# Kernel optimization log

Hardware: AMD Instinct MI355X
Metric: run time of the kernel (lower is better)

Reference implementation:

```python
import jax, jax.numpy as jnp
import numpy as np

TEMPERATURE = 0.7
BIG_NEG = -1e30  # safe stand-in for -inf (keeps grads finite)


def setup_inputs() -> dict:
    key = jax.random.key(0)
    k1, k2, k3 = jax.random.split(key, 3)
    B, D = 8192, 256
    embeddings = jax.random.normal(k1, (B, D), dtype=jnp.float32)
    categories = jax.random.randint(k2, (B,), 0, 16, dtype=jnp.int64)
    font_labels = jax.random.randint(k3, (B,), 0, 2000, dtype=jnp.int64)
    return {"embeddings": embeddings, "categories": categories, "font_labels": font_labels}


def reference(embeddings, categories, font_labels):
    # L2-normalize rows
    e = embeddings / jnp.linalg.norm(embeddings, axis=1, keepdims=True)
    sims = jnp.matmul(e, e.T) / TEMPERATURE  # [B, B]
    B = sims.shape[0]

    same = categories[:, None] == categories[None, :]
    diag = jnp.eye(B, dtype=bool)
    pos_mask = same & ~diag           # same category, excluding self
    neg_mask = ~same                  # different category (self excluded implicitly)

    valid = pos_mask.any(axis=1) & neg_mask.any(axis=1)

    pos_sim = jnp.max(jnp.where(pos_mask, sims, BIG_NEG), axis=1)  # hardest positive per anchor
    neg_max = jnp.max(jnp.where(neg_mask, sims, BIG_NEG), axis=1)

    # logsumexp over {pos_sim} U neg_sims, numerically stable
    m = jnp.where(valid, jnp.maximum(pos_sim, neg_max), 0.0)
    pos_safe = jnp.where(valid, pos_sim, 0.0)
    exp_neg_sum = jnp.sum(jnp.where(neg_mask, jnp.exp(sims - m[:, None]), 0.0), axis=1)
    lse = m + jnp.log(jnp.exp(pos_safe - m) + exp_neg_sum)

    loss_per_anchor = -pos_safe + lse
    n_valid = jnp.maximum(jnp.sum(valid), 1)
    return jnp.sum(jnp.where(valid, loss_per_anchor, 0.0)) / n_valid
```

## Files before the change

### kernel.cpp

```cpp
#include <hip/hip_runtime.h>
#include <stdint.h>

#define NROWS 8192
#define DDIM 256
#define NSTRIPS 32
#define STRIP_COLS 256
#define BN 32
#define NTILES 8
#define BM 128
#define NSLOT NSTRIPS

#define ESCALE 1.4356159f
#define LN2F   0.6931471806f
#define NEGBIG (-1e30f)

typedef __attribute__((ext_vector_type(8))) short short8;
typedef __attribute__((ext_vector_type(4))) float f32x4;

__device__ __forceinline__ unsigned short f2bf(float x) {
  unsigned int u = __float_as_uint(x);
  u += 0x7fffu + ((u >> 16) & 1u);
  return (unsigned short)(u >> 16);
}

__global__ __launch_bounds__(256) void knorm(const float* __restrict__ emb,
                                             unsigned short* __restrict__ ebf,
                                             unsigned short* __restrict__ ebfB,
                                             uint4* __restrict__ accv) {
  if (blockIdx.x == 0 && threadIdx.x == 0) *accv = (uint4){0u, 0u, 0u, 0u};
  const int wave = threadIdx.x >> 6, lane = threadIdx.x & 63;
  const int row = blockIdx.x * 4 + wave;
  const float4 v = *(const float4*)(emb + row * DDIM + lane * 4);
  float ss = v.x * v.x + v.y * v.y + v.z * v.z + v.w * v.w;
#pragma unroll
  for (int off = 1; off < 64; off <<= 1) ss += __shfl_xor(ss, off, 64);
  const float sc = rsqrtf(ss) * ESCALE;
  ushort4 o;
  o.x = f2bf(v.x * sc); o.y = f2bf(v.y * sc);
  o.z = f2bf(v.z * sc); o.w = f2bf(v.w * sc);
  *(ushort4*)(ebf + row * DDIM + lane * 4) = o;
  *(ushort4*)(ebfB + ((lane >> 1) * NROWS + row) * 8 + (lane & 1) * 4) = o;
}

__global__ __launch_bounds__(256) void kmain(const unsigned short* __restrict__ ebf,
                                             const unsigned short* __restrict__ ebfB,
                                             const int* __restrict__ cats,
                                             float* __restrict__ posP,
                                             float* __restrict__ sumP) {
  const int tid = threadIdx.x;
  const int lane = tid & 63, wave = tid >> 6;
  const int lane15 = lane & 15, quad = lane >> 4;
  const int strip = blockIdx.x, rowTile = blockIdx.y;
  const int rowG = rowTile * BM + wave * 32;
  const int col0 = strip * STRIP_COLS;

  short8 a[2][8];
#pragma unroll
  for (int m = 0; m < 2; ++m)
#pragma unroll
    for (int kk = 0; kk < 8; ++kk)
      a[m][kk] = *(const short8*)(ebf + (rowG + m * 16 + lane15) * DDIM + kk * 32 + quad * 8);

  int cati[2][4];
#pragma unroll
  for (int m = 0; m < 2; ++m)
#pragma unroll
    for (int r = 0; r < 4; ++r)
      cati[m][r] = cats[rowG + m * 16 + quad * 4 + r];

  bool dlr[4];
#pragma unroll
  for (int r = 0; r < 4; ++r) dlr[r] = (lane15 == quad * 4 + r);

  float pm[2][4], ns[2][4];
#pragma unroll
  for (int m = 0; m < 2; ++m)
#pragma unroll
    for (int r = 0; r < 4; ++r) { pm[m][r] = NEGBIG; ns[m][r] = 0.f; }

  const unsigned short* bbase = ebfB + ((size_t)quad * NROWS + col0 + lane15) * 8;

  for (int t = 0; t < NTILES; ++t) {
#pragma unroll
    for (int nt = 0; nt < 2; ++nt) {
      const int colBase = col0 + t * BN + nt * 16;
      short8 b[8];
#pragma unroll
      for (int kk = 0; kk < 8; ++kk)
        b[kk] = *(const short8*)(bbase + ((size_t)kk * 4 * NROWS + t * BN + nt * 16) * 8);
      f32x4 acc0 = {0.f, 0.f, 0.f, 0.f}, acc1 = {0.f, 0.f, 0.f, 0.f};
      __builtin_amdgcn_s_setprio(1);
#pragma unroll
      for (int kk = 0; kk < 8; ++kk) {
        acc0 = __builtin_amdgcn_mfma_f32_16x16x32_bf16(a[0][kk], b[kk], acc0, 0, 0, 0);
        acc1 = __builtin_amdgcn_mfma_f32_16x16x32_bf16(a[1][kk], b[kk], acc1, 0, 0, 0);
      }
      __builtin_amdgcn_s_setprio(0);
      const int cj = cats[colBase + lane15];
      const bool dg0 = (rowG == colBase);
      const bool dg1 = (rowG + 16 == colBase);
#pragma unroll
      for (int m = 0; m < 2; ++m) {
        const bool dg = m ? dg1 : dg0;
#pragma unroll
        for (int r = 0; r < 4; ++r) {
          const float s = m ? acc1[r] : acc0[r];
          const float e = __builtin_amdgcn_exp2f(s);
          const bool same = (cj == cati[m][r]);
          float psv = same ? s : NEGBIG;
          if (dg) psv = dlr[r] ? NEGBIG : psv;
          pm[m][r] = fmaxf(pm[m][r], psv);
          ns[m][r] += same ? 0.f : e;
        }
      }
    }
  }

#pragma unroll
  for (int off = 1; off < 16; off <<= 1) {
#pragma unroll
    for (int m = 0; m < 2; ++m)
#pragma unroll
      for (int r = 0; r < 4; ++r) {
        pm[m][r] = fmaxf(pm[m][r], __shfl_xor(pm[m][r], off, 64));
        ns[m][r] += __shfl_xor(ns[m][r], off, 64);
      }
  }
  if (lane15 == 0) {
#pragma unroll
    for (int m = 0; m < 2; ++m)
#pragma unroll
      for (int r = 0; r < 4; ++r) {
        const int row = rowG + m * 16 + quad * 4 + r;
        posP[strip * NROWS + row] = pm[m][r];
        sumP[strip * NROWS + row] = ns[m][r];
      }
  }
}

__global__ __launch_bounds__(256) void kmerge(const float* __restrict__ posP,
                                              const float* __restrict__ sumP,
                                              float* __restrict__ acc,
                                              float* __restrict__ out) {
  const int row = blockIdx.x * 256 + threadIdx.x;
  float pm = NEGBIG, ns = 0.f;
#pragma unroll 8
  for (int s = 0; s < NSLOT; ++s) {
    pm = fmaxf(pm, posP[s * NROWS + row]);
    ns += sumP[s * NROWS + row];
  }
  const bool valid = (pm > -1e29f) && (ns > 0.f);
  float loss = valid ? (logf(__builtin_amdgcn_exp2f(pm) + ns) - pm * LN2F) : 0.f;
  float cnt = valid ? 1.f : 0.f;
#pragma unroll
  for (int off = 1; off < 64; off <<= 1) {
    loss += __shfl_xor(loss, off, 64);
    cnt += __shfl_xor(cnt, off, 64);
  }
  if ((threadIdx.x & 63) == 0) {
    atomicAdd(&acc[0], loss);
    atomicAdd(&acc[1], cnt);
    __threadfence();
  }
  __syncthreads();
  if (threadIdx.x == 0) {
    const int prev = atomicAdd((int*)(acc + 2), 1);
    if (prev == (int)gridDim.x - 1) {
      const float L = atomicAdd(&acc[0], 0.f);
      const float C = atomicAdd(&acc[1], 0.f);
      out[0] = L / fmaxf(C, 1.f);
    }
  }
}

extern "C" void kernel_launch(void* const* d_in, const int* in_sizes, int n_in,
                              void* d_out, int out_size, void* d_ws, size_t ws_size,
                              hipStream_t stream) {
  const float* emb = (const float*)d_in[0];
  const int* cats = (const int*)d_in[1];
  float* out = (float*)d_out;

  char* ws = (char*)d_ws;
  float* accv = (float*)ws;
  unsigned short* ebf = (unsigned short*)(ws + 256);
  unsigned short* ebfB = ebf + (size_t)NROWS * DDIM;
  float* posP = (float*)(ws + 256 + 2 * (size_t)NROWS * DDIM * 2);
  float* sumP = posP + NSLOT * NROWS;

  knorm<<<NROWS / 4, 256, 0, stream>>>(emb, ebf, ebfB, (uint4*)ws);
  kmain<<<dim3(NSTRIPS, NROWS / BM), 256, 0, stream>>>(ebf, ebfB, cats, posP, sumP);
  kmerge<<<NROWS / 256, 256, 0, stream>>>(posP, sumP, accv, out);
}
```

Baseline: 121.1 us.

## Double-buffer B fragment loads and drop row-major bf16 copy

```diff
diff --git a/kernel.cpp b/kernel.cpp
--- a/kernel.cpp
+++ b/kernel.cpp
@@ -24,7 +24,6 @@
 }
 
 __global__ __launch_bounds__(256) void knorm(const float* __restrict__ emb,
-                                             unsigned short* __restrict__ ebf,
                                              unsigned short* __restrict__ ebfB,
                                              uint4* __restrict__ accv) {
   if (blockIdx.x == 0 && threadIdx.x == 0) *accv = (uint4){0u, 0u, 0u, 0u};
@@ -38,18 +37,17 @@
   ushort4 o;
   o.x = f2bf(v.x * sc); o.y = f2bf(v.y * sc);
   o.z = f2bf(v.z * sc); o.w = f2bf(v.w * sc);
-  *(ushort4*)(ebf + row * DDIM + lane * 4) = o;
   *(ushort4*)(ebfB + ((lane >> 1) * NROWS + row) * 8 + (lane & 1) * 4) = o;
 }
 
-__global__ __launch_bounds__(256) void kmain(const unsigned short* __restrict__ ebf,
-                                             const unsigned short* __restrict__ ebfB,
+__global__ __launch_bounds__(256) void kmain(const unsigned short* __restrict__ ebfB,
                                              const int* __restrict__ cats,
                                              float* __restrict__ posP,
                                              float* __restrict__ sumP) {
   const int tid = threadIdx.x;
-  const int lane = tid & 63, wave = tid >> 6;
+  const int lane = tid & 63;
   const int lane15 = lane & 15, quad = lane >> 4;
+  const int wave = tid >> 6;
   const int strip = blockIdx.x, rowTile = blockIdx.y;
   const int rowG = rowTile * BM + wave * 32;
   const int col0 = strip * STRIP_COLS;
@@ -59,7 +57,8 @@
   for (int m = 0; m < 2; ++m)
 #pragma unroll
     for (int kk = 0; kk < 8; ++kk)
-      a[m][kk] = *(const short8*)(ebf + (rowG + m * 16 + lane15) * DDIM + kk * 32 + quad * 8);
+      a[m][kk] = *(const short8*)(ebfB +
+          ((size_t)(kk * 4 + quad) * NROWS + rowG + m * 16 + lane15) * 8);
 
   int cati[2][4];
 #pragma unroll
@@ -80,40 +79,50 @@
 
   const unsigned short* bbase = ebfB + ((size_t)quad * NROWS + col0 + lane15) * 8;
 
+#define LOADB(buf, t, nt)                                                       \
+  _Pragma("unroll")                                                             \
+  for (int kk = 0; kk < 8; ++kk)                                                \
+    buf[kk] = *(const short8*)(bbase +                                          \
+        ((size_t)kk * 4 * NROWS + (t) * BN + (nt) * 16) * 8);
+
+#define DOMFMA(buf, ACC0, ACC1)                                                 \
+  f32x4 ACC0 = {0.f, 0.f, 0.f, 0.f}, ACC1 = {0.f, 0.f, 0.f, 0.f};              \
+  _Pragma("unroll")                                                             \
+  for (int kk = 0; kk < 8; ++kk) {                                              \
+    ACC0 = __builtin_amdgcn_mfma_f32_16x16x32_bf16(a[0][kk], buf[kk], ACC0, 0, 0, 0); \
+    ACC1 = __builtin_amdgcn_mfma_f32_16x16x32_bf16(a[1][kk], buf[kk], ACC1, 0, 0, 0); \
+  }
+
+#define EPI(ACC0, ACC1, t, nt)                                                  \
+  {                                                                             \
+    const int colBase = col0 + (t) * BN + (nt) * 16;                            \
+    const int cj = cats[colBase + lane15];                                      \
+    const bool dg0 = (rowG == colBase);                                         \
+    const bool dg1 = (rowG + 16 == colBase);                                    \
+    _Pragma("unroll")                                                           \
+    for (int m = 0; m < 2; ++m) {                                               \
+      const bool dg = m ? dg1 : dg0;                                            \
+      _Pragma("unroll")                                                         \
+      for (int r = 0; r < 4; ++r) {                                             \
+        const float s = m ? ACC1[r] : ACC0[r];         \
+        const float e = __builtin_amdgcn_exp2f(s);                              \
+        const bool same = (cj == cati[m][r]);                                   \
+        float psv = same ? s : NEGBIG;                                          \
+        if (dg) psv = dlr[r] ? NEGBIG : psv;           \
+        pm[m][r] = fmaxf(pm[m][r], psv);                                        \
+        ns[m][r] += same ? 0.f : e;                                             \
+      }                                                                         \
+    }                                                                           \
+  }
+
+  short8 b0[8], b1[8];
+  LOADB(b0, 0, 0);
+
   for (int t = 0; t < NTILES; ++t) {
-#pragma unroll
-    for (int nt = 0; nt < 2; ++nt) {
-      const int colBase = col0 + t * BN + nt * 16;
-      short8 b[8];
-#pragma unroll
-      for (int kk = 0; kk < 8; ++kk)
-        b[kk] = *(const short8*)(bbase + ((size_t)kk * 4 * NROWS + t * BN + nt * 16) * 8);
-      f32x4 acc0 = {0.f, 0.f, 0.f, 0.f}, acc1 = {0.f, 0.f, 0.f, 0.f};
-      __builtin_amdgcn_s_setprio(1);
-#pragma unroll
-      for (int kk = 0; kk < 8; ++kk) {
-        acc0 = __builtin_amdgcn_mfma_f32_16x16x32_bf16(a[0][kk], b[kk], acc0, 0, 0, 0);
-        acc1 = __builtin_amdgcn_mfma_f32_16x16x32_bf16(a[1][kk], b[kk], acc1, 0, 0, 0);
-      }
-      __builtin_amdgcn_s_setprio(0);
-      const int cj = cats[colBase + lane15];
-      const bool dg0 = (rowG == colBase);
-      const bool dg1 = (rowG + 16 == colBase);
-#pragma unroll
-      for (int m = 0; m < 2; ++m) {
-        const bool dg = m ? dg1 : dg0;
-#pragma unroll
-        for (int r = 0; r < 4; ++r) {
-          const float s = m ? acc1[r] : acc0[r];
-          const float e = __builtin_amdgcn_exp2f(s);
-          const bool same = (cj == cati[m][r]);
-          float psv = same ? s : NEGBIG;
-          if (dg) psv = dlr[r] ? NEGBIG : psv;
-          pm[m][r] = fmaxf(pm[m][r], psv);
-          ns[m][r] += same ? 0.f : e;
-        }
-      }
-    }
+    LOADB(b1, t, 1);
+    { DOMFMA(b0, acc0, acc1) EPI(acc0, acc1, t, 0) }
+    if (t + 1 < NTILES) LOADB(b0, t + 1, 0);
+    { DOMFMA(b1, acc2, acc3) EPI(acc2, acc3, t, 1) }
   }
 
 #pragma unroll
@@ -182,12 +191,11 @@
 
   char* ws = (char*)d_ws;
   float* accv = (float*)ws;
-  unsigned short* ebf = (unsigned short*)(ws + 256);
-  unsigned short* ebfB = ebf + (size_t)NROWS * DDIM;
-  float* posP = (float*)(ws + 256 + 2 * (size_t)NROWS * DDIM * 2);
+  unsigned short* ebfB = (unsigned short*)(ws + 256);
+  float* posP = (float*)(ws + 256 + (size_t)NROWS * DDIM * 2);
   float* sumP = posP + NSLOT * NROWS;
 
-  knorm<<<NROWS / 4, 256, 0, stream>>>(emb, ebf, ebfB, (uint4*)ws);
-  kmain<<<dim3(NSTRIPS, NROWS / BM), 256, 0, stream>>>(ebf, ebfB, cats, posP, sumP);
+  knorm<<<NROWS / 4, 256, 0, stream>>>(emb, ebfB, (uint4*)ws);
+  kmain<<<dim3(NSTRIPS, NROWS / BM), 256, 0, stream>>>(ebfB, cats, posP, sumP);
   kmerge<<<NROWS / 256, 256, 0, stream>>>(posP, sumP, accv, out);
 }
```

After: 114.8 us. -5.2%, faster.
